# Optimization experiments

Measured on AMD Instinct MI355X. Metric: run time of the kernel, lower is better.

Reference implementation:

```python
import jax, jax.numpy as jnp
import numpy as np

N = 50000   # total residue nodes across the batch of peptides
E = 800000  # total directed intra-peptide edges (avg degree 16)
D = 512


def _w(k, shape):
    fan_in = shape[0]
    return (jax.random.normal(k, shape, jnp.float32) / np.sqrt(fan_in)).astype(jnp.float32)


def setup_inputs() -> dict:
    key = jax.random.key(0)
    ks = jax.random.split(key, 12)
    return {
        "peptide_feature": jax.random.normal(ks[0], (N, D), jnp.float32),
        "edge_index": jax.random.randint(ks[1], (2, E), 0, N),
        # aanet_proj: 512 -> 1024 -> 1024 -> 512 -> 80 (ReLU between, none after last)
        "W1": _w(ks[2], (512, 1024)), "b1": jnp.zeros((1024,), jnp.float32),
        "W2": _w(ks[3], (1024, 1024)), "b2": jnp.zeros((1024,), jnp.float32),
        "W3": _w(ks[4], (1024, 512)), "b3": jnp.zeros((512,), jnp.float32),
        "W4": _w(ks[5], (512, 80)), "b4": jnp.zeros((80,), jnp.float32),
        # in_net: 80 -> 512
        "Win": _w(ks[6], (80, 512)), "bin_": jnp.zeros((512,), jnp.float32),
        # GIN conv MLP: 512 -> 512 -> 512 (eps = 0)
        "Wg1": _w(ks[7], (512, 512)), "bg1": jnp.zeros((512,), jnp.float32),
        "Wg2": _w(ks[8], (512, 512)), "bg2": jnp.zeros((512,), jnp.float32),
        # out_net: 512 -> 80
        "Wout": _w(ks[9], (512, 80)), "bout": jnp.zeros((80,), jnp.float32),
    }


def reference(peptide_feature, edge_index, W1, b1, W2, b2, W3, b3, W4, b4,
              Win, bin_, Wg1, bg1, Wg2, bg2, Wout, bout):
    relu = jax.nn.relu
    # aanet_proj
    h = relu(peptide_feature @ W1 + b1)
    h = relu(h @ W2 + b2)
    h = relu(h @ W3 + b3)
    peptide_feat = h @ W4 + b4                      # [N, 80]
    # in_net
    x = peptide_feat @ Win + bin_                   # [N, 512]
    # GIN message passing (sum aggregation, eps=0): per-sample loop in the
    # original is equivalent to one global pass since edges are sample-local.
    src, dst = edge_index[0], edge_index[1]
    agg = jax.ops.segment_sum(x[src], dst, num_segments=N)   # [N, 512]
    g = x + agg
    g = relu(g @ Wg1 + bg1) @ Wg2 + bg2             # GIN MLP
    # out_net
    peptide_mask = g @ Wout + bout                  # [N, 80]
    return peptide_mask, peptide_feat
```

## Files before the change

kernel.cpp:

```cpp
#include <hip/hip_runtime.h>
#include <stdint.h>


using bf16x8 = __attribute__((ext_vector_type(8))) short;
using f32x4  = __attribute__((ext_vector_type(4))) float;

__device__ inline unsigned short f2bf(float f) {
    union { float f; unsigned u; } v; v.f = f;
    unsigned u = v.u;
    u += 0x7FFFu + ((u >> 16) & 1u);
    return (unsigned short)(u >> 16);
}
__device__ inline float bf2f(unsigned u16) {
    return __uint_as_float(u16 << 16);
}

struct PreDescs {
    const float* W[8]; unsigned short* Wt[8];
    int K[8], M[8], Kp[8], ntx[8], start[8];
    int tEnd, cEnd, eEnd;
    const float* feat; unsigned short* featb; int nFeat;
    const int* ei; int E; int* cnt; int* rank;
};

__global__ __launch_bounds__(256) void rg_preprocess(PreDescs d) {
    int b = blockIdx.x;
    int tid = threadIdx.x;
    if (b < d.tEnd) {
        __shared__ float t[32][33];
        int di = 0;
#pragma unroll
        for (int i = 1; i < 8; ++i) if (b >= d.start[i]) di = i;
        int local = b - d.start[di];
        int bx = local % d.ntx[di];
        int by = local / d.ntx[di];
        const float* W = d.W[di];
        unsigned short* Wt = d.Wt[di];
        int K = d.K[di], M = d.M[di], Kp = d.Kp[di];
        int mb = bx * 32, kb = by * 32;
        int tx = tid & 31, tg = tid >> 5;
#pragma unroll
        for (int p = 0; p < 4; ++p) {
            int r = tg + p * 8;
            int k = kb + r, m = mb + tx;
            t[r][tx] = (k < K && m < M) ? W[(size_t)k * M + m] : 0.f;
        }
        __syncthreads();
#pragma unroll
        for (int p = 0; p < 4; ++p) {
            int r = tg + p * 8;
            int mo = mb + r, ko = kb + tx;
            Wt[(size_t)mo * Kp + ko] = f2bf(t[tx][r]);
        }
    } else if (b < d.cEnd) {
        int base = (b - d.tEnd) * 4096 + tid * 4;
#pragma unroll
        for (int p = 0; p < 4; ++p) {
            int i = base + p * 1024;
            if (i + 3 < d.nFeat) {
                float4 v = *(const float4*)(d.feat + i);
                ushort4 o; o.x = f2bf(v.x); o.y = f2bf(v.y); o.z = f2bf(v.z); o.w = f2bf(v.w);
                *(ushort4*)(d.featb + i) = o;
            }
        }
    } else {
        int e0 = (b - d.cEnd) * 1024 + tid;
#pragma unroll
        for (int p = 0; p < 4; ++p) {
            int e = e0 + p * 256;
            if (e < d.E) {
                int dd = d.ei[d.E + e];
                d.rank[e] = atomicAdd(&d.cnt[dd], 1);
            }
        }
    }
}

template <bool RELU, bool OUT_BF, bool OUT_F32, bool DEGB, int MT>
__device__ __forceinline__ void gemm_body(
    int bid,
    const unsigned short* __restrict__ A, const unsigned short* __restrict__ Bt,
    const float* __restrict__ bias, const int* __restrict__ deg, int Mvalid,
    unsigned short* __restrict__ outB, float* __restrict__ outF,
    int Nrows, int Kp, int Mp, int gN)
{
    __shared__ __align__(16) unsigned short As[128 * 64];
    __shared__ __align__(16) unsigned short Bs[128 * 64];

    int xcd = bid & 7;
    int slot = bid >> 3;
    int c = slot % MT;
    int rsub = slot / MT;
    int rt = rsub * 8 + xcd;
    if (rt >= gN) return;
    const int rowBase = rt * 128;
    const int nBase   = c * 128;

    const int tid  = threadIdx.x;
    const int lane = tid & 63;
    const int w    = tid >> 6;
    const int wm   = w & 1, wn = w >> 1;

    f32x4 acc[4][4];
#pragma unroll
    for (int i = 0; i < 4; ++i)
#pragma unroll
        for (int j = 0; j < 4; ++j) acc[i][j] = (f32x4){0.f, 0.f, 0.f, 0.f};

    const int nkt = Kp >> 6;
    for (int kt = 0; kt < nkt; ++kt) {
        __syncthreads();
        const int k0 = kt * 64;
#pragma unroll
        for (int i = 0; i < 4; ++i) {
            int q   = i * 256 + tid;
            int r   = q >> 3;
            int cbg = (q & 7) ^ (r & 7);
            const unsigned short* gp = A + (size_t)(rowBase + r) * Kp + k0 + cbg * 8;
            __builtin_amdgcn_global_load_lds(
                (const __attribute__((address_space(1))) void*)gp,
                (__attribute__((address_space(3))) void*)(&As[q * 8]), 16, 0, 0);
        }
#pragma unroll
        for (int i = 0; i < 4; ++i) {
            int q   = i * 256 + tid;
            int r   = q >> 3;
            int cbg = (q & 7) ^ (r & 7);
            const unsigned short* gp = Bt + (size_t)(nBase + r) * Kp + k0 + cbg * 8;
            __builtin_amdgcn_global_load_lds(
                (const __attribute__((address_space(1))) void*)gp,
                (__attribute__((address_space(3))) void*)(&Bs[q * 8]), 16, 0, 0);
        }
        __syncthreads();
#pragma unroll
        for (int kk = 0; kk < 2; ++kk) {
            bf16x8 a[4], b[4];
            const int cb = kk * 4 + (lane >> 4);
#pragma unroll
            for (int i = 0; i < 4; ++i) {
                int r = wm * 64 + i * 16 + (lane & 15);
                a[i] = *(const bf16x8*)&As[(r * 8 + (cb ^ (r & 7))) * 8];
            }
#pragma unroll
            for (int j = 0; j < 4; ++j) {
                int r = wn * 64 + j * 16 + (lane & 15);
                b[j] = *(const bf16x8*)&Bs[(r * 8 + (cb ^ (r & 7))) * 8];
            }
#pragma unroll
            for (int i = 0; i < 4; ++i)
#pragma unroll
                for (int j = 0; j < 4; ++j)
                    acc[i][j] = __builtin_amdgcn_mfma_f32_16x16x32_bf16(b[j], a[i], acc[i][j], 0, 0, 0);
        }
    }

    const int quad = lane >> 4;
#pragma unroll
    for (int i = 0; i < 4; ++i) {
        int row = rowBase + wm * 64 + i * 16 + (lane & 15);
        if (row >= Nrows) continue;
        float sc = 1.f;
        if (DEGB) sc = 1.f + (float)deg[row];
#pragma unroll
        for (int j = 0; j < 4; ++j) {
            int colb = nBase + wn * 64 + j * 16 + quad * 4;
            float4 bv = (colb < Mvalid) ? *(const float4*)(bias + colb)
                                        : (float4){0.f, 0.f, 0.f, 0.f};
            float v0 = acc[i][j][0] + sc * bv.x;
            float v1 = acc[i][j][1] + sc * bv.y;
            float v2 = acc[i][j][2] + sc * bv.z;
            float v3 = acc[i][j][3] + sc * bv.w;
            if (RELU) {
                v0 = v0 > 0.f ? v0 : 0.f; v1 = v1 > 0.f ? v1 : 0.f;
                v2 = v2 > 0.f ? v2 : 0.f; v3 = v3 > 0.f ? v3 : 0.f;
            }
            if (OUT_BF) {
                ushort4 o; o.x = f2bf(v0); o.y = f2bf(v1); o.z = f2bf(v2); o.w = f2bf(v3);
                *(ushort4*)(outB + (size_t)row * Mp + colb) = o;
            }
            if (OUT_F32) {
                if (colb < Mvalid)
                    *(float4*)(outF + (size_t)row * Mvalid + colb) = (float4){v0, v1, v2, v3};
            }
        }
    }
}

template <bool RELU, bool OUT_BF, bool OUT_F32, bool DEGB, int MT>
__global__ __launch_bounds__(256, 4) void rg_gemm(
    const unsigned short* __restrict__ A, const unsigned short* __restrict__ Bt,
    const float* __restrict__ bias, const int* __restrict__ deg, int Mvalid,
    unsigned short* __restrict__ outB, float* __restrict__ outF,
    int Nrows, int Kp, int Mp, int gN)
{
    gemm_body<RELU, OUT_BF, OUT_F32, DEGB, MT>(blockIdx.x, A, Bt, bias, deg,
                                               Mvalid, outB, outF, Nrows, Kp, Mp, gN);
}

template <bool RELU, bool OUT_BF, bool OUT_F32, int MT>
__global__ __launch_bounds__(256, 4) void rg_gemm64(
    const unsigned short* __restrict__ A, const unsigned short* __restrict__ Bt,
    const float* __restrict__ bias, int Mvalid,
    unsigned short* __restrict__ outB, float* __restrict__ outF,
    int Nrows, int Kp, int Mp, int gN64)
{
    __shared__ __align__(16) unsigned short As[64 * 64];
    __shared__ __align__(16) unsigned short Bs[128 * 64];

    int bid = blockIdx.x;
    int xcd = bid & 7;
    int slot = bid >> 3;
    int c = slot % MT;
    int rsub = slot / MT;
    int rt = rsub * 8 + xcd;
    if (rt >= gN64) return;
    const int rowBase = rt * 64;
    const int nBase   = c * 128;

    const int tid  = threadIdx.x;
    const int lane = tid & 63;
    const int wn   = tid >> 6;

    f32x4 acc[4][2];
#pragma unroll
    for (int i = 0; i < 4; ++i)
#pragma unroll
        for (int j = 0; j < 2; ++j) acc[i][j] = (f32x4){0.f, 0.f, 0.f, 0.f};

    const int nkt = Kp >> 6;
    for (int kt = 0; kt < nkt; ++kt) {
        __syncthreads();
        const int k0 = kt * 64;
#pragma unroll
        for (int i = 0; i < 2; ++i) {
            int q   = i * 256 + tid;
            int r   = q >> 3;
            int cbg = (q & 7) ^ (r & 7);
            const unsigned short* gp = A + (size_t)(rowBase + r) * Kp + k0 + cbg * 8;
            __builtin_amdgcn_global_load_lds(
                (const __attribute__((address_space(1))) void*)gp,
                (__attribute__((address_space(3))) void*)(&As[q * 8]), 16, 0, 0);
        }
#pragma unroll
        for (int i = 0; i < 4; ++i) {
            int q   = i * 256 + tid;
            int r   = q >> 3;
            int cbg = (q & 7) ^ (r & 7);
            const unsigned short* gp = Bt + (size_t)(nBase + r) * Kp + k0 + cbg * 8;
            __builtin_amdgcn_global_load_lds(
                (const __attribute__((address_space(1))) void*)gp,
                (__attribute__((address_space(3))) void*)(&Bs[q * 8]), 16, 0, 0);
        }
        __syncthreads();
#pragma unroll
        for (int kk = 0; kk < 2; ++kk) {
            bf16x8 a[4], b[2];
            const int cb = kk * 4 + (lane >> 4);
#pragma unroll
            for (int i = 0; i < 4; ++i) {
                int r = i * 16 + (lane & 15);
                a[i] = *(const bf16x8*)&As[(r * 8 + (cb ^ (r & 7))) * 8];
            }
#pragma unroll
            for (int j = 0; j < 2; ++j) {
                int r = wn * 32 + j * 16 + (lane & 15);
                b[j] = *(const bf16x8*)&Bs[(r * 8 + (cb ^ (r & 7))) * 8];
            }
#pragma unroll
            for (int i = 0; i < 4; ++i)
#pragma unroll
                for (int j = 0; j < 2; ++j)
                    acc[i][j] = __builtin_amdgcn_mfma_f32_16x16x32_bf16(b[j], a[i], acc[i][j], 0, 0, 0);
        }
    }

    const int quad = lane >> 4;
#pragma unroll
    for (int i = 0; i < 4; ++i) {
        int row = rowBase + i * 16 + (lane & 15);
        if (row >= Nrows) continue;
#pragma unroll
        for (int j = 0; j < 2; ++j) {
            int colb = nBase + wn * 32 + j * 16 + quad * 4;
            float4 bv = (colb < Mvalid) ? *(const float4*)(bias + colb)
                                        : (float4){0.f, 0.f, 0.f, 0.f};
            float v0 = acc[i][j][0] + bv.x;
            float v1 = acc[i][j][1] + bv.y;
            float v2 = acc[i][j][2] + bv.z;
            float v3 = acc[i][j][3] + bv.w;
            if (RELU) {
                v0 = v0 > 0.f ? v0 : 0.f; v1 = v1 > 0.f ? v1 : 0.f;
                v2 = v2 > 0.f ? v2 : 0.f; v3 = v3 > 0.f ? v3 : 0.f;
            }
            if (OUT_BF) {
                ushort4 o; o.x = f2bf(v0); o.y = f2bf(v1); o.z = f2bf(v2); o.w = f2bf(v3);
                *(ushort4*)(outB + (size_t)row * Mp + colb) = o;
            }
            if (OUT_F32) {
                if (colb < Mvalid)
                    *(float4*)(outF + (size_t)row * Mvalid + colb) = (float4){v0, v1, v2, v3};
            }
        }
    }
}

__global__ __launch_bounds__(256, 4) void rg_gemm_l1_scatter(
    const unsigned short* __restrict__ A, const unsigned short* __restrict__ Bt,
    const float* __restrict__ bias, int Mvalid,
    unsigned short* __restrict__ outB, int Nrows, int Kp, int Mp, int gN,
    int gemmBlocks, const int* __restrict__ ei, int E,
    const int* __restrict__ rowptr, const int* __restrict__ rank,
    int* __restrict__ cols)
{
    int bid = blockIdx.x;
    if (bid < gemmBlocks) {
        gemm_body<true, true, false, false, 8>(bid, A, Bt, bias, nullptr,
                                               Mvalid, outB, nullptr, Nrows, Kp, Mp, gN);
    } else {
        int e = (bid - gemmBlocks) * 256 + threadIdx.x;
        if (e < E) {
            int d = ei[E + e];
            int p = rowptr[d] + rank[e];
            cols[p] = ei[e];
        }
    }
}

__device__ __forceinline__ void rg_gridbar(int* bar, int nb, int phase) {
    __syncthreads();
    if (threadIdx.x == 0) {
        __threadfence();
        atomicAdd(bar, 1);
        int target = phase * nb;
        while (__hip_atomic_load(bar, __ATOMIC_RELAXED, __HIP_MEMORY_SCOPE_AGENT) < target) {}
        __threadfence();
    }
    __syncthreads();
}

__global__ __launch_bounds__(1024) void rg_scan_all(
    const int* __restrict__ cnt, int* __restrict__ rowptr,
    int* __restrict__ bsums, int* bar, int Nn, int E, int nb)
{
    __shared__ int sd[1024];
    const int tid = threadIdx.x;
    const int bid = blockIdx.x;
    const int i   = bid * 1024 + tid;

    int v = (i < Nn) ? cnt[i] : 0;
    sd[tid] = v;
    __syncthreads();
    for (int off = 1; off < 1024; off <<= 1) {
        int t = (tid >= off) ? sd[tid - off] : 0;
        __syncthreads();
        sd[tid] += t;
        __syncthreads();
    }
    if (tid == 1023) bsums[bid] = sd[1023];
    rg_gridbar(bar, nb, 1);

    if (bid == 0 && tid < 64) {
        int bv = (tid < nb) ? bsums[tid] : 0;
        int incl = bv;
#pragma unroll
        for (int off = 1; off < 64; off <<= 1) {
            int t = __shfl_up(incl, off, 64);
            if (tid >= off) incl += t;
        }
        if (tid < nb) bsums[tid] = incl - bv;
    }
    rg_gridbar(bar, nb, 2);

    if (i < Nn) {
        int ex = sd[tid] - v + bsums[bid];
        rowptr[i] = ex;
    }
    if (i == 0) rowptr[Nn] = E;
}

__global__ __launch_bounds__(256) void rg_agg80(
    const unsigned short* __restrict__ pf, const int* __restrict__ rowptr,
    const int* __restrict__ cols, unsigned short* __restrict__ s, int Nn)
{
    int node = blockIdx.x * 4 + (threadIdx.x >> 6);
    if (node >= Nn) return;
    int lane = threadIdx.x & 63;
    const unsigned* xp = (const unsigned*)pf;
    size_t off = (size_t)node * 64 + lane;
    unsigned u = xp[off];
    float a0 = bf2f(u & 0xffffu), a1 = bf2f(u >> 16);
    int beg = rowptr[node], end = rowptr[node + 1];
    int e = beg;
    for (; e + 8 <= end; e += 8) {
        unsigned v[8];
#pragma unroll
        for (int t = 0; t < 8; ++t) v[t] = xp[(size_t)cols[e + t] * 64 + lane];
#pragma unroll
        for (int t = 0; t < 8; ++t) { a0 += bf2f(v[t] & 0xffffu); a1 += bf2f(v[t] >> 16); }
    }
    for (; e < end; ++e) {
        unsigned v = xp[(size_t)cols[e] * 64 + lane];
        a0 += bf2f(v & 0xffffu); a1 += bf2f(v >> 16);
    }
    unsigned o = (unsigned)f2bf(a0) | ((unsigned)f2bf(a1) << 16);
    ((unsigned*)s)[off] = o;
}

extern "C" void kernel_launch(void* const* d_in, const int* in_sizes, int n_in,
                              void* d_out, int out_size, void* d_ws, size_t ws_size,
                              hipStream_t stream)
{
    const float* feat = (const float*)d_in[0];
    const int*   ei   = (const int*)d_in[1];
    const float* W1 = (const float*)d_in[2];  const float* b1 = (const float*)d_in[3];
    const float* W2 = (const float*)d_in[4];  const float* b2 = (const float*)d_in[5];
    const float* W3 = (const float*)d_in[6];  const float* b3 = (const float*)d_in[7];
    const float* W4 = (const float*)d_in[8];  const float* b4 = (const float*)d_in[9];
    const float* Wi = (const float*)d_in[10]; const float* bi = (const float*)d_in[11];
    const float* Wg1 = (const float*)d_in[12]; const float* bg1 = (const float*)d_in[13];
    const float* Wg2 = (const float*)d_in[14]; const float* bg2 = (const float*)d_in[15];
    const float* Wo = (const float*)d_in[16]; const float* bo = (const float*)d_in[17];

    const int N = in_sizes[0] / 512;
    const int E = in_sizes[1] / 2;
    const int gN = (N + 127) / 128;
    const int Npad = gN * 128;

    char* ws = (char*)d_ws;
    size_t o = 0;
    auto alloc = [&](size_t bytes) { char* p = ws + o; o += (bytes + 255) & ~(size_t)255; return p; };
    unsigned short* bufA = (unsigned short*)alloc((size_t)Npad * 1024 * 2);
    unsigned short* bufB = (unsigned short*)alloc((size_t)Npad * 1024 * 2);
    unsigned short* bufC = (unsigned short*)alloc((size_t)Npad * 512 * 2);
    unsigned short* W1t = (unsigned short*)alloc((size_t)1024 * 512 * 2);
    unsigned short* W2t = (unsigned short*)alloc((size_t)1024 * 1024 * 2);
    unsigned short* W3t = (unsigned short*)alloc((size_t)512 * 1024 * 2);
    unsigned short* W4t = (unsigned short*)alloc((size_t)128 * 512 * 2);
    unsigned short* Wit = (unsigned short*)alloc((size_t)512 * 128 * 2);
    unsigned short* Wg1t = (unsigned short*)alloc((size_t)512 * 512 * 2);
    unsigned short* Wg2t = (unsigned short*)alloc((size_t)512 * 512 * 2);
    unsigned short* Wot = (unsigned short*)alloc((size_t)128 * 512 * 2);
    int* cnt    = (int*)alloc((size_t)(N + 64) * 4);
    int* bar    = cnt + N;
    int* rowptr = (int*)alloc((size_t)(N + 1) * 4);
    int* rank   = (int*)alloc((size_t)E * 4);
    int* cols   = (int*)alloc((size_t)E * 4);
    int* bsums  = (int*)alloc(256);

    float* out_mask = (float*)d_out;
    float* out_feat = (float*)d_out + (size_t)N * 80;

    hipMemsetAsync(cnt, 0, (size_t)(N + 64) * 4, stream);
    {
        PreDescs d;
        const float* Ws[8]  = {W1, W2, W3, W4, Wi, Wg1, Wg2, Wo};
        unsigned short* Ts[8] = {W1t, W2t, W3t, W4t, Wit, Wg1t, Wg2t, Wot};
        int Ks[8]  = {512, 1024, 1024, 512, 80, 512, 512, 512};
        int Ms[8]  = {1024, 1024, 512, 80, 512, 512, 512, 80};
        int Kps[8] = {512, 1024, 1024, 512, 128, 512, 512, 512};
        int Mps[8] = {1024, 1024, 512, 128, 512, 512, 512, 128};
        int st = 0;
        for (int i = 0; i < 8; ++i) {
            d.W[i] = Ws[i]; d.Wt[i] = Ts[i];
            d.K[i] = Ks[i]; d.M[i] = Ms[i]; d.Kp[i] = Kps[i];
            d.ntx[i] = Mps[i] / 32;
            d.start[i] = st;
            st += (Mps[i] / 32) * (Kps[i] / 32);
        }
        d.tEnd = st;
        d.cEnd = st + (N * 512) / 4096;
        d.eEnd = d.cEnd + (E + 1023) / 1024;
        d.feat = feat; d.featb = bufC; d.nFeat = N * 512;
        d.ei = ei; d.E = E; d.cnt = cnt; d.rank = rank;
        rg_preprocess<<<d.eEnd, 256, 0, stream>>>(d);
    }

    const int nb = (N + 1023) / 1024;
    rg_scan_all<<<nb, 1024, 0, stream>>>(cnt, rowptr, bsums, bar, N, E, nb);

    const int rg8 = ((gN + 7) / 8) * 8;
    auto grid = [&](int MT) { return dim3(rg8 * MT); };
    const int gN64 = (N + 63) / 64;
    const int rg64 = ((gN64 + 7) / 8) * 8;

    {
        const int gemmBlocks = rg8 * 8;
        const int scatBlocks = (E + 255) / 256;
        rg_gemm_l1_scatter<<<dim3(gemmBlocks + scatBlocks), 256, 0, stream>>>(
            bufC, W1t, b1, 1024, bufA, N, 512, 1024, gN,
            gemmBlocks, ei, E, rowptr, rank, cols);
    }

    rg_gemm<true, true, false, false, 8><<<grid(8), 256, 0, stream>>>(bufA, W2t, b2, nullptr, 1024, bufB, nullptr, N, 1024, 1024, gN);
    rg_gemm<true, true, false, false, 4><<<grid(4), 256, 0, stream>>>(bufB, W3t, b3, nullptr, 512, bufC, nullptr, N, 1024, 512, gN);
    rg_gemm64<false, true, true, 1><<<dim3(rg64), 256, 0, stream>>>(bufC, W4t, b4, 80, bufA, out_feat, N, 512, 128, gN64);

    rg_agg80<<<(N + 3) / 4, 256, 0, stream>>>(bufA, rowptr, cols, bufC, N);

    rg_gemm<false, true, false, true, 4><<<grid(4), 256, 0, stream>>>(bufC, Wit, bi, cnt, 512, bufA, nullptr, N, 128, 512, gN);
    rg_gemm<true, true, false, false, 4><<<grid(4), 256, 0, stream>>>(bufA, Wg1t, bg1, nullptr, 512, bufB, nullptr, N, 512, 512, gN);
    rg_gemm<false, true, false, false, 4><<<grid(4), 256, 0, stream>>>(bufB, Wg2t, bg2, nullptr, 512, bufC, nullptr, N, 512, 512, gN);
    rg_gemm64<false, false, true, 1><<<dim3(rg64), 256, 0, stream>>>(bufC, Wot, bo, 80, nullptr, out_mask, N, 512, 128, gN64);
}
```

Before: 702.2 us.

## Add 256x256-tile 8-wave pipelined GEMM for the 1024x1024 layer

Adds a new bf16 MFMA GEMM kernel with 256x256 output tiles, 512 threads and double-buffered LDS filled by direct global-to-LDS loads. Each K step is split into four phases that interleave the next tile's loads with MFMA work, using explicit barriers and waitcnts. It replaces the previous 128-wide tile kernel for the W2 layer only. The larger tile raises data reuse per load, but it uses more LDS and registers, which lowers occupancy, and the hand-written synchronisation has to stay correct.

```diff
diff --git a/kernel.cpp b/kernel.cpp
--- a/kernel.cpp
+++ b/kernel.cpp
@@ -195,6 +195,178 @@
 {
     gemm_body<RELU, OUT_BF, OUT_F32, DEGB, MT>(blockIdx.x, A, Bt, bias, deg,
                                                Mvalid, outB, outF, Nrows, Kp, Mp, gN);
+}
+
+template <bool RELU, int MT>
+__global__ __launch_bounds__(512, 2) void rg_gemm256_8ph(
+    const unsigned short* __restrict__ A, const unsigned short* __restrict__ Bt,
+    const float* __restrict__ bias, unsigned short* __restrict__ outB,
+    int Nrows, int NrowsPad, int Kp, int Mp, int gN2)
+{
+    __shared__ __align__(16) unsigned short As[2][2][128 * 64];
+    __shared__ __align__(16) unsigned short Bs[2][2][128 * 64];
+
+    int bid = blockIdx.x;
+    int xcd = bid & 7;
+    int slotb = bid >> 3;
+    int c = slotb % MT;
+    int rsub = slotb / MT;
+    int rt = rsub * 8 + xcd;
+    if (rt >= gN2) return;
+    const int rowBase = rt * 256;
+    const int nBase   = c * 256;
+
+    const int tid  = threadIdx.x;
+    const int lane = tid & 63;
+    const int w    = tid >> 6;
+    const int wm   = w & 1;
+    const int wn   = w >> 1;
+    const int hb   = wn >> 1;
+    const int wc   = wn & 1;
+    const int lane15 = lane & 15;
+    const int laneq  = lane >> 4;
+
+    f32x4 acc[8][4];
+#pragma unroll
+    for (int i = 0; i < 8; ++i)
+#pragma unroll
+        for (int j = 0; j < 4; ++j) acc[i][j] = (f32x4){0.f, 0.f, 0.f, 0.f};
+
+    const int nkt = Kp >> 6;
+
+    auto stageA = [&](int t, int hf) {
+        const int k0 = t << 6;
+        unsigned short* dst = &As[t & 1][hf][0];
+#pragma unroll
+        for (int ld = 0; ld < 2; ++ld) {
+            int q   = ld * 512 + tid;
+            int r   = q >> 3;
+            int cbg = (q & 7) ^ (r & 7);
+            int grow = rowBase + hf * 128 + r;
+            grow = grow < NrowsPad ? grow : NrowsPad - 1;
+            const unsigned short* gp = A + (size_t)grow * Kp + k0 + cbg * 8;
+            __builtin_amdgcn_global_load_lds(
+                (const __attribute__((address_space(1))) void*)gp,
+                (__attribute__((address_space(3))) void*)(dst + q * 8), 16, 0, 0);
+        }
+    };
+    auto stageB = [&](int t, int hf) {
+        const int k0 = t << 6;
+        unsigned short* dst = &Bs[t & 1][hf][0];
+#pragma unroll
+        for (int ld = 0; ld < 2; ++ld) {
+            int q   = ld * 512 + tid;
+            int r   = q >> 3;
+            int cbg = (q & 7) ^ (r & 7);
+            const unsigned short* gp = Bt + (size_t)(nBase + hf * 128 + r) * Kp + k0 + cbg * 8;
+            __builtin_amdgcn_global_load_lds(
+                (const __attribute__((address_space(1))) void*)gp,
+                (__attribute__((address_space(3))) void*)(dst + q * 8), 16, 0, 0);
+        }
+    };
+
+    bf16x8 av[4][2];
+    bf16x8 bv0[2][2], bv1[2][2];
+
+    auto readA = [&](int slot, int rh) {
+#pragma unroll
+        for (int i = 0; i < 4; ++i) {
+            int lr = rh * 64 + i * 16 + lane15;
+#pragma unroll
+            for (int kk = 0; kk < 2; ++kk) {
+                int cb = kk * 4 + laneq;
+                av[i][kk] = *(const bf16x8*)&As[slot][wm][(lr * 8 + (cb ^ (lr & 7))) * 8];
+            }
+        }
+    };
+    auto readB = [&](int slot, int ch, bf16x8 bv[2][2]) {
+#pragma unroll
+        for (int j = 0; j < 2; ++j) {
+            int lc = wc * 64 + ch * 32 + j * 16 + lane15;
+#pragma unroll
+            for (int kk = 0; kk < 2; ++kk) {
+                int cb = kk * 4 + laneq;
+                bv[j][kk] = *(const bf16x8*)&Bs[slot][hb][(lc * 8 + (cb ^ (lc & 7))) * 8];
+            }
+        }
+    };
+    auto mfma16 = [&](int rh, int ch, bf16x8 bv[2][2]) {
+        __builtin_amdgcn_s_setprio(1);
+#pragma unroll
+        for (int i = 0; i < 4; ++i)
+#pragma unroll
+            for (int j = 0; j < 2; ++j)
+#pragma unroll
+                for (int kk = 0; kk < 2; ++kk)
+                    acc[rh * 4 + i][ch * 2 + j] = __builtin_amdgcn_mfma_f32_16x16x32_bf16(
+                        bv[j][kk], av[i][kk], acc[rh * 4 + i][ch * 2 + j], 0, 0, 0);
+        __builtin_amdgcn_s_setprio(0);
+    };
+
+#define RG_SYNC_IN  do { __builtin_amdgcn_sched_barrier(0); __builtin_amdgcn_s_barrier(); \
+                         asm volatile("s_waitcnt lgkmcnt(0)" ::: "memory"); \
+                         __builtin_amdgcn_sched_barrier(0); } while (0)
+#define RG_SYNC_OUT do { __builtin_amdgcn_sched_barrier(0); __builtin_amdgcn_s_barrier(); } while (0)
+
+    stageA(0, 0); stageB(0, 0); stageB(0, 1); stageA(0, 1);
+    stageB(1, 0); stageB(1, 1);
+    asm volatile("s_waitcnt vmcnt(4)" ::: "memory");
+    __builtin_amdgcn_sched_barrier(0);
+    __builtin_amdgcn_s_barrier();
+    __builtin_amdgcn_sched_barrier(0);
+
+    for (int a = 0; a < nkt; ++a) {
+        const int slot = a & 1;
+        readA(slot, 0);
+        readB(slot, 0, bv0);
+        if (a + 1 < nkt) stageA(a + 1, 0);
+        RG_SYNC_IN;
+        mfma16(0, 0, bv0);
+        RG_SYNC_OUT;
+        readB(slot, 1, bv1);
+        if (a + 1 < nkt) stageA(a + 1, 1);
+        RG_SYNC_IN;
+        mfma16(0, 1, bv1);
+        RG_SYNC_OUT;
+        readA(slot, 1);
+        if (a + 2 < nkt) stageB(a + 2, 0);
+        RG_SYNC_IN;
+        mfma16(1, 0, bv0);
+        RG_SYNC_OUT;
+        if (a + 2 < nkt) {
+            stageB(a + 2, 1);
+            asm volatile("s_waitcnt vmcnt(4)" ::: "memory");
+        } else if (a + 1 < nkt) {
+            asm volatile("s_waitcnt vmcnt(0)" ::: "memory");
+        }
+        RG_SYNC_IN;
+        mfma16(1, 1, bv1);
+        RG_SYNC_OUT;
+    }
+#undef RG_SYNC_IN
+#undef RG_SYNC_OUT
+
+    const int quad = lane >> 4;
+#pragma unroll
+    for (int mi = 0; mi < 8; ++mi) {
+        int row = rowBase + wm * 128 + mi * 16 + lane15;
+        if (row >= Nrows) continue;
+#pragma unroll
+        for (int nj = 0; nj < 4; ++nj) {
+            int colb = nBase + wn * 64 + nj * 16 + quad * 4;
+            float4 bvv = *(const float4*)(bias + colb);
+            float v0 = acc[mi][nj][0] + bvv.x;
+            float v1 = acc[mi][nj][1] + bvv.y;
+            float v2 = acc[mi][nj][2] + bvv.z;
+            float v3 = acc[mi][nj][3] + bvv.w;
+            if (RELU) {
+                v0 = v0 > 0.f ? v0 : 0.f; v1 = v1 > 0.f ? v1 : 0.f;
+                v2 = v2 > 0.f ? v2 : 0.f; v3 = v3 > 0.f ? v3 : 0.f;
+            }
+            ushort4 o; o.x = f2bf(v0); o.y = f2bf(v1); o.z = f2bf(v2); o.w = f2bf(v3);
+            *(ushort4*)(outB + (size_t)row * Mp + colb) = o;
+        }
+    }
 }
 
 template <bool RELU, bool OUT_BF, bool OUT_F32, int MT>
@@ -482,6 +654,8 @@
     auto grid = [&](int MT) { return dim3(rg8 * MT); };
     const int gN64 = (N + 63) / 64;
     const int rg64 = ((gN64 + 7) / 8) * 8;
+    const int gN2 = (N + 255) / 256;
+    const int rg256 = ((gN2 + 7) / 8) * 8;
 
     {
         const int gemmBlocks = rg8 * 8;
@@ -491,7 +665,7 @@
             gemmBlocks, ei, E, rowptr, rank, cols);
     }
 
-    rg_gemm<true, true, false, false, 8><<<grid(8), 256, 0, stream>>>(bufA, W2t, b2, nullptr, 1024, bufB, nullptr, N, 1024, 1024, gN);
+    rg_gemm256_8ph<true, 4><<<dim3(rg256 * 4), 512, 0, stream>>>(bufA, W2t, b2, bufB, N, Npad, 1024, 1024, gN2);
     rg_gemm<true, true, false, false, 4><<<grid(4), 256, 0, stream>>>(bufB, W3t, b3, nullptr, 512, bufC, nullptr, N, 1024, 512, gN);
     rg_gemm64<false, true, true, 1><<<dim3(rg64), 256, 0, stream>>>(bufC, W4t, b4, 80, bufA, out_feat, N, 512, 128, gN64);
 
```

Result: slower. 721.4 us (+2.7%).

## Fuse neighbor aggregation into the in_net GEMM via shared-memory A tile

Applied to the files above, without the earlier changes.

Replaces the separate 80-dim aggregation kernel and the following in_net GEMM with one kernel. Each block gathers and sums neighbor features for its 128 rows directly into a swizzled LDS A tile, then runs the 128->512 MFMA GEMM from LDS with degree-scaled bias. This removes the global write and re-read of the aggregated tensor and one launch. In exchange, each block now does a serial per-node gather loop (32 rows per wave) before any MFMA work, and there are fewer blocks (one per row tile instead of four), which may reduce parallelism in the gather phase.

```diff
diff --git a/kernel.cpp b/kernel.cpp
--- a/kernel.cpp
+++ b/kernel.cpp
@@ -304,6 +304,128 @@
     }
 }
 
+__global__ __launch_bounds__(256, 4) void rg_agg_gemm_l5(
+    const unsigned short* __restrict__ pf,
+    const int* __restrict__ rowptr, const int* __restrict__ cols,
+    const unsigned short* __restrict__ Bt,
+    const float* __restrict__ bias, const int* __restrict__ deg,
+    unsigned short* __restrict__ outB,
+    int Nn, int gN)
+{
+    __shared__ __align__(16) unsigned short AsK[2][128 * 64];
+    __shared__ __align__(16) unsigned short Bs[128 * 64];
+
+    int bid = blockIdx.x;
+    int xcd = bid & 7;
+    int rsub = bid >> 3;
+    int rt = rsub * 8 + xcd;
+    if (rt >= gN) return;
+    const int rowBase = rt * 128;
+
+    const int tid  = threadIdx.x;
+    const int lane = tid & 63;
+    const int w    = tid >> 6;
+
+    {
+        const unsigned* xp = (const unsigned*)pf;
+        const int t    = lane >> 5;
+        const int lc   = lane & 31;
+        const int cbg  = lc >> 2;
+        const int upos = lc & 3;
+        for (int rr = 0; rr < 32; ++rr) {
+            int lr = w * 32 + rr;
+            int node = rowBase + lr;
+            if (node < Nn) {
+                size_t off = (size_t)node * 64 + lane;
+                unsigned u = xp[off];
+                float a0 = bf2f(u & 0xffffu), a1 = bf2f(u >> 16);
+                int beg = rowptr[node], end = rowptr[node + 1];
+                int e = beg;
+                for (; e + 8 <= end; e += 8) {
+                    unsigned v[8];
+#pragma unroll
+                    for (int p = 0; p < 8; ++p) v[p] = xp[(size_t)cols[e + p] * 64 + lane];
+#pragma unroll
+                    for (int p = 0; p < 8; ++p) { a0 += bf2f(v[p] & 0xffffu); a1 += bf2f(v[p] >> 16); }
+                }
+                for (; e < end; ++e) {
+                    unsigned v = xp[(size_t)cols[e] * 64 + lane];
+                    a0 += bf2f(v & 0xffffu); a1 += bf2f(v >> 16);
+                }
+                unsigned o = (unsigned)f2bf(a0) | ((unsigned)f2bf(a1) << 16);
+                int q = lr * 8 + (cbg ^ (lr & 7));
+                ((unsigned*)AsK[t])[q * 4 + upos] = o;
+            }
+        }
+    }
+    __syncthreads();
+
+    const int wm = w & 1, wn = w >> 1;
+    const int quad = lane >> 4;
+    for (int c = 0; c < 4; ++c) {
+        f32x4 acc[4][4];
+#pragma unroll
+        for (int i = 0; i < 4; ++i)
+#pragma unroll
+            for (int j = 0; j < 4; ++j) acc[i][j] = (f32x4){0.f, 0.f, 0.f, 0.f};
+
+#pragma unroll
+        for (int kt = 0; kt < 2; ++kt) {
+            __syncthreads();
+            const int k0 = kt * 64;
+#pragma unroll
+            for (int i = 0; i < 4; ++i) {
+                int q   = i * 256 + tid;
+                int r   = q >> 3;
+                int cb2 = (q & 7) ^ (r & 7);
+                const unsigned short* gp = Bt + (size_t)(c * 128 + r) * 128 + k0 + cb2 * 8;
+                __builtin_amdgcn_global_load_lds(
+                    (const __attribute__((address_space(1))) void*)gp,
+                    (__attribute__((address_space(3))) void*)(&Bs[q * 8]), 16, 0, 0);
+            }
+            __syncthreads();
+#pragma unroll
+            for (int kk = 0; kk < 2; ++kk) {
+                bf16x8 a[4], b[4];
+                const int cb = kk * 4 + (lane >> 4);
+#pragma unroll
+                for (int i = 0; i < 4; ++i) {
+                    int r = wm * 64 + i * 16 + (lane & 15);
+                    a[i] = *(const bf16x8*)&AsK[kt][(r * 8 + (cb ^ (r & 7))) * 8];
+                }
+#pragma unroll
+                for (int j = 0; j < 4; ++j) {
+                    int r = wn * 64 + j * 16 + (lane & 15);
+                    b[j] = *(const bf16x8*)&Bs[(r * 8 + (cb ^ (r & 7))) * 8];
+                }
+#pragma unroll
+                for (int i = 0; i < 4; ++i)
+#pragma unroll
+                    for (int j = 0; j < 4; ++j)
+                        acc[i][j] = __builtin_amdgcn_mfma_f32_16x16x32_bf16(b[j], a[i], acc[i][j], 0, 0, 0);
+            }
+        }
+
+#pragma unroll
+        for (int i = 0; i < 4; ++i) {
+            int row = rowBase + wm * 64 + i * 16 + (lane & 15);
+            if (row >= Nn) continue;
+            float sc = 1.f + (float)deg[row];
+#pragma unroll
+            for (int j = 0; j < 4; ++j) {
+                int colb = c * 128 + wn * 64 + j * 16 + quad * 4;
+                float4 bv = *(const float4*)(bias + colb);
+                float v0 = acc[i][j][0] + sc * bv.x;
+                float v1 = acc[i][j][1] + sc * bv.y;
+                float v2 = acc[i][j][2] + sc * bv.z;
+                float v3 = acc[i][j][3] + sc * bv.w;
+                ushort4 o; o.x = f2bf(v0); o.y = f2bf(v1); o.z = f2bf(v2); o.w = f2bf(v3);
+                *(ushort4*)(outB + (size_t)row * 512 + colb) = o;
+            }
+        }
+    }
+}
+
 __global__ __launch_bounds__(256, 4) void rg_gemm_l1_scatter(
     const unsigned short* __restrict__ A, const unsigned short* __restrict__ Bt,
     const float* __restrict__ bias, int Mvalid,
@@ -376,34 +498,6 @@
         rowptr[i] = ex;
     }
     if (i == 0) rowptr[Nn] = E;
-}
-
-__global__ __launch_bounds__(256) void rg_agg80(
-    const unsigned short* __restrict__ pf, const int* __restrict__ rowptr,
-    const int* __restrict__ cols, unsigned short* __restrict__ s, int Nn)
-{
-    int node = blockIdx.x * 4 + (threadIdx.x >> 6);
-    if (node >= Nn) return;
-    int lane = threadIdx.x & 63;
-    const unsigned* xp = (const unsigned*)pf;
-    size_t off = (size_t)node * 64 + lane;
-    unsigned u = xp[off];
-    float a0 = bf2f(u & 0xffffu), a1 = bf2f(u >> 16);
-    int beg = rowptr[node], end = rowptr[node + 1];
-    int e = beg;
-    for (; e + 8 <= end; e += 8) {
-        unsigned v[8];
-#pragma unroll
-        for (int t = 0; t < 8; ++t) v[t] = xp[(size_t)cols[e + t] * 64 + lane];
-#pragma unroll
-        for (int t = 0; t < 8; ++t) { a0 += bf2f(v[t] & 0xffffu); a1 += bf2f(v[t] >> 16); }
-    }
-    for (; e < end; ++e) {
-        unsigned v = xp[(size_t)cols[e] * 64 + lane];
-        a0 += bf2f(v & 0xffffu); a1 += bf2f(v >> 16);
-    }
-    unsigned o = (unsigned)f2bf(a0) | ((unsigned)f2bf(a1) << 16);
-    ((unsigned*)s)[off] = o;
 }
 
 extern "C" void kernel_launch(void* const* d_in, const int* in_sizes, int n_in,
@@ -495,10 +589,9 @@
     rg_gemm<true, true, false, false, 4><<<grid(4), 256, 0, stream>>>(bufB, W3t, b3, nullptr, 512, bufC, nullptr, N, 1024, 512, gN);
     rg_gemm64<false, true, true, 1><<<dim3(rg64), 256, 0, stream>>>(bufC, W4t, b4, 80, bufA, out_feat, N, 512, 128, gN64);
 
-    rg_agg80<<<(N + 3) / 4, 256, 0, stream>>>(bufA, rowptr, cols, bufC, N);
-
-    rg_gemm<false, true, false, true, 4><<<grid(4), 256, 0, stream>>>(bufC, Wit, bi, cnt, 512, bufA, nullptr, N, 128, 512, gN);
-    rg_gemm<true, true, false, false, 4><<<grid(4), 256, 0, stream>>>(bufA, Wg1t, bg1, nullptr, 512, bufB, nullptr, N, 512, 512, gN);
-    rg_gemm<false, true, false, false, 4><<<grid(4), 256, 0, stream>>>(bufB, Wg2t, bg2, nullptr, 512, bufC, nullptr, N, 512, 512, gN);
+    rg_agg_gemm_l5<<<dim3(rg8), 256, 0, stream>>>(bufA, rowptr, cols, Wit, bi, cnt, bufB, N, gN);
+
+    rg_gemm<true, true, false, false, 4><<<grid(4), 256, 0, stream>>>(bufB, Wg1t, bg1, nullptr, 512, bufA, nullptr, N, 512, 512, gN);
+    rg_gemm<false, true, false, false, 4><<<grid(4), 256, 0, stream>>>(bufA, Wg2t, bg2, nullptr, 512, bufC, nullptr, N, 512, 512, gN);
     rg_gemm64<false, false, true, 1><<<dim3(rg64), 256, 0, stream>>>(bufC, Wot, bo, 80, nullptr, out_mask, N, 512, 128, gN64);
 }
```

New measurement: 768.4 us. 9.4% more time.
